# Optimization experiments

Hardware: AMD Instinct MI355X
Metric: run time of the kernel (lower is better)

## Reference

```python
import jax, jax.numpy as jnp
import numpy as np

B, S, D, H = 128, 1024, 512, 512


def setup_inputs() -> dict:
    key = jax.random.key(0)
    ks = jax.random.split(key, 8)
    return {
        "input": jax.random.normal(ks[0], (B, D), jnp.float32),
        "context": jax.random.normal(ks[1], (B, S, D), jnp.float32),
        "mask": jax.random.randint(ks[2], (B, S), 0, 2).astype(bool),
        "W_in": jax.random.normal(ks[3], (H, D), jnp.float32) * (1.0 / np.sqrt(D)),
        "b_in": jax.random.normal(ks[4], (H,), jnp.float32) * 0.01,
        "W_ctx": jax.random.normal(ks[5], (H, D), jnp.float32) * (1.0 / np.sqrt(D)),
        "b_ctx": jax.random.normal(ks[6], (H,), jnp.float32) * 0.01,
        "V": jax.random.uniform(ks[7], (H,), jnp.float32, -1.0, 1.0),
    }


def reference(input, context, mask, W_in, b_in, W_ctx, b_ctx, V):
    # inp: [B, H] -> broadcast over S (torch: unsqueeze(2).expand)
    inp = input @ W_in.T + b_in
    # 1x1 Conv1d over permuted context == per-position linear: [B, H, S]
    ctx = jnp.einsum('bsd,hd->bhs', context, W_ctx) + b_ctx[None, :, None]
    # additive (Bahdanau) score: V . tanh(inp + ctx) over H -> [B, S]
    att = jnp.einsum('h,bhs->bs', V, jnp.tanh(inp[:, :, None] + ctx))
    att = jnp.where(mask, -jnp.inf, att)
    alpha = jax.nn.softmax(att, axis=-1)  # [B, S]
    # weighted sum of projected context: [B, H]
    hidden_state = jnp.einsum('bhs,bs->bh', ctx, alpha)
    return (hidden_state, alpha)
```

## Files before the change

### kernel.cpp

```cpp
#include <hip/hip_runtime.h>
#include <math.h>

#define B_ 128
#define S_ 1024
#define D_ 512
#define H_ 512

typedef _Float16 f16x4 __attribute__((ext_vector_type(4)));
typedef _Float16 f16x8 __attribute__((ext_vector_type(8)));
typedef float    f32x4 __attribute__((ext_vector_type(4)));

__global__ void zero_k(float* __restrict__ p, int n) {
    int i = blockIdx.x * 256 + threadIdx.x;
    if (i < n) p[i] = 0.f;
}

__global__ void init2_k(float* __restrict__ att, float* __restrict__ hidden,
                        const float* __restrict__ bc) {
    int i = blockIdx.x * 256 + threadIdx.x;
    if (i < B_ * S_) att[i] = 0.f;
    else if (i < B_ * S_ + B_ * H_) {
        int j = i - B_ * S_;
        hidden[j] = bc[j & (H_ - 1)];
    }
}

__global__ __launch_bounds__(256) void linear_k(const float* __restrict__ X,
                                                const float* __restrict__ W,
                                                const float* __restrict__ bias,
                                                float* __restrict__ out) {
    int idx = blockIdx.x * 256 + threadIdx.x;
    int b = idx >> 9;
    int h = idx & 511;
    const float4* x = (const float4*)(X + (size_t)b * D_);
    const float4* w = (const float4*)(W + (size_t)h * D_);
    float s = 0.f;
#pragma unroll 8
    for (int k = 0; k < D_ / 4; ++k) {
        float4 xv = x[k], wv = w[k];
        s = fmaf(xv.x, wv.x, s);
        s = fmaf(xv.y, wv.y, s);
        s = fmaf(xv.z, wv.z, s);
        s = fmaf(xv.w, wv.w, s);
    }
    out[idx] = s + bias[h];
}

__device__ inline f16x8 cvt8(float4 a, float4 b) {
    f16x8 r;
    r[0] = (_Float16)a.x; r[1] = (_Float16)a.y;
    r[2] = (_Float16)a.z; r[3] = (_Float16)a.w;
    r[4] = (_Float16)b.x; r[5] = (_Float16)b.y;
    r[6] = (_Float16)b.z; r[7] = (_Float16)b.w;
    return r;
}

__device__ inline float fast_tanh(float x) {
    float e = __expf(2.f * x);
    return 1.f - 2.f / (e + 1.f);
}

template <bool WCTX>
__global__ __launch_bounds__(256) void score_mfma(const float* __restrict__ ctx,
                                                  const float* __restrict__ Wc,
                                                  const float* __restrict__ bc,
                                                  const float* __restrict__ Vv,
                                                  const float* __restrict__ inp,
                                                  float* __restrict__ att,
                                                  _Float16* __restrict__ ctxp) {
    __shared__ __align__(16) _Float16 Ah[2][128][32];
    __shared__ __align__(16) _Float16 Bh[2][128][32];
    __shared__ float red[8][128];

    const int tid = threadIdx.x;
    const int s0 = blockIdx.x * 128;
    const int h0 = blockIdx.y * 128;
    const int b  = blockIdx.z;

    const int r0  = tid >> 2;
    const int kg  = tid & 3;
    const int swz = ((kg ^ (r0 & 3)) << 3);

    const int wave = tid >> 6;
    const int lane = tid & 63;
    const int wm = wave >> 1, wn = wave & 1;
    const int l15 = lane & 15, quad = lane >> 4;
    const int rdsw = ((quad ^ (l15 & 3)) << 3);

    const float* Arow0 = Wc  + (size_t)(h0 + r0) * D_ + kg * 8;
    const float* Arow1 = Arow0 + (size_t)64 * D_;
    const float* Brow0 = ctx + ((size_t)b * S_ + s0 + r0) * D_ + kg * 8;
    const float* Brow1 = Brow0 + (size_t)64 * D_;

    f32x4 acc[4][4];
#pragma unroll
    for (int mi = 0; mi < 4; ++mi)
#pragma unroll
        for (int ni = 0; ni < 4; ++ni) acc[mi][ni] = (f32x4){0.f, 0.f, 0.f, 0.f};

    float4 A0a, A0b, A1a, A1b, B0a, B0b, B1a, B1b;

#define LOADS(step) do { const int kk_ = (step) * 32;                               \
    A0a = *(const float4*)(Arow0 + kk_); A0b = *(const float4*)(Arow0 + kk_ + 4);   \
    A1a = *(const float4*)(Arow1 + kk_); A1b = *(const float4*)(Arow1 + kk_ + 4);   \
    B0a = *(const float4*)(Brow0 + kk_); B0b = *(const float4*)(Brow0 + kk_ + 4);   \
    B1a = *(const float4*)(Brow1 + kk_); B1b = *(const float4*)(Brow1 + kk_ + 4); } while (0)

#define WRITE(bf) do {                                                              \
    *(f16x8*)&Ah[bf][r0][swz]      = cvt8(A0a, A0b);                                \
    *(f16x8*)&Ah[bf][r0 + 64][swz] = cvt8(A1a, A1b);                                \
    *(f16x8*)&Bh[bf][r0][swz]      = cvt8(B0a, B0b);                                \
    *(f16x8*)&Bh[bf][r0 + 64][swz] = cvt8(B1a, B1b); } while (0)

#define COMPUTE(bf) do {                                                            \
    f16x8 bhf_[4];                                                                  \
    _Pragma("unroll")                                                               \
    for (int ni = 0; ni < 4; ++ni)                                                  \
        bhf_[ni] = *(const f16x8*)&Bh[bf][wn * 64 + ni * 16 + l15][rdsw];           \
    _Pragma("unroll")                                                               \
    for (int mi = 0; mi < 4; ++mi) {                                                \
        f16x8 ah_ = *(const f16x8*)&Ah[bf][wm * 64 + mi * 16 + l15][rdsw];          \
        _Pragma("unroll")                                                           \
        for (int ni = 0; ni < 4; ++ni)                                              \
            acc[mi][ni] = __builtin_amdgcn_mfma_f32_16x16x32_f16(ah_, bhf_[ni],     \
                                                                 acc[mi][ni], 0, 0, 0); \
    } } while (0)

    LOADS(0);
    WRITE(0);
    LOADS(1);
    __syncthreads();

    for (int it = 0; it < 16; it += 2) {
        COMPUTE(0);
        WRITE(1);
        if (it + 2 < 16) LOADS(it + 2);
        __syncthreads();
        COMPUTE(1);
        if (it + 2 < 16) WRITE(0);
        if (it + 3 < 16) LOADS(it + 3);
        __syncthreads();
    }
#undef LOADS
#undef WRITE
#undef COMPUTE

    if (WCTX) {
#pragma unroll
        for (int ni = 0; ni < 4; ++ni) {
            const size_t srow = ((size_t)b * S_ + s0 + wn * 64 + ni * 16 + l15) * H_;
#pragma unroll
            for (int mi = 0; mi < 4; ++mi) {
                f16x4 v;
                v[0] = (_Float16)acc[mi][ni][0];
                v[1] = (_Float16)acc[mi][ni][1];
                v[2] = (_Float16)acc[mi][ni][2];
                v[3] = (_Float16)acc[mi][ni][3];
                *(f16x4*)(ctxp + srow + h0 + wm * 64 + mi * 16 + quad * 4) = v;
            }
        }
    }

    float p[4] = {0.f, 0.f, 0.f, 0.f};
#pragma unroll
    for (int mi = 0; mi < 4; ++mi) {
#pragma unroll
        for (int r = 0; r < 4; ++r) {
            const int h = h0 + wm * 64 + mi * 16 + quad * 4 + r;
            const float c  = inp[(size_t)b * H_ + h] + bc[h];
            const float vh = Vv[h];
#pragma unroll
            for (int ni = 0; ni < 4; ++ni)
                p[ni] = fmaf(vh, fast_tanh(c + acc[mi][ni][r]), p[ni]);
        }
    }
    const int cid = wm * 4 + quad;
#pragma unroll
    for (int ni = 0; ni < 4; ++ni)
        red[cid][wn * 64 + ni * 16 + l15] = p[ni];
    __syncthreads();
    if (tid < 128) {
        float s = 0.f;
#pragma unroll
        for (int g = 0; g < 8; ++g) s += red[g][tid];
        atomicAdd(att + (size_t)b * S_ + s0 + tid, s);
    }
}

__global__ __launch_bounds__(256) void softmax_k(const float* __restrict__ att,
                                                 const int* __restrict__ mask,
                                                 float* __restrict__ alpha) {
    const int b = blockIdx.x;
    const int t = threadIdx.x;
    __shared__ float sm[256];
    float v[4];
    float mx = -INFINITY;
#pragma unroll
    for (int i = 0; i < 4; ++i) {
        int s = t + i * 256;
        float a = att[(size_t)b * S_ + s];
        int mk = mask[(size_t)b * S_ + s];
        v[i] = mk ? -INFINITY : a;
        mx = fmaxf(mx, v[i]);
    }
    sm[t] = mx;
    __syncthreads();
    for (int off = 128; off > 0; off >>= 1) {
        if (t < off) sm[t] = fmaxf(sm[t], sm[t + off]);
        __syncthreads();
    }
    mx = sm[0];
    __syncthreads();
    float e[4];
    float sum = 0.f;
#pragma unroll
    for (int i = 0; i < 4; ++i) {
        e[i] = expf(v[i] - mx);
        sum += e[i];
    }
    sm[t] = sum;
    __syncthreads();
    for (int off = 128; off > 0; off >>= 1) {
        if (t < off) sm[t] += sm[t + off];
        __syncthreads();
    }
    float inv = 1.f / sm[0];
#pragma unroll
    for (int i = 0; i < 4; ++i) alpha[(size_t)b * S_ + t + i * 256] = e[i] * inv;
}

__global__ __launch_bounds__(256) void cbar2_k(const _Float16* __restrict__ ctxp,
                                               const float* __restrict__ alpha,
                                               float* __restrict__ hidden) {
    const int b  = blockIdx.y;
    const int s0 = blockIdx.x * 128;
    const int t  = threadIdx.x;
    const int w = t >> 6, lane = t & 63;
    __shared__ float al[128];
    __shared__ float red[3][512];
    if (t < 128) al[t] = alpha[(size_t)b * S_ + s0 + t];
    __syncthreads();
    const _Float16* base = ctxp + ((size_t)b * S_ + s0) * H_ + lane * 8;
    float acc[8] = {0.f, 0.f, 0.f, 0.f, 0.f, 0.f, 0.f, 0.f};
#pragma unroll 4
    for (int s = w; s < 128; s += 4) {
        float a = al[s];
        f16x8 v = *(const f16x8*)(base + (size_t)s * H_);
#pragma unroll
        for (int j = 0; j < 8; ++j) acc[j] = fmaf(a, (float)v[j], acc[j]);
    }
    if (w > 0) {
#pragma unroll
        for (int j = 0; j < 8; ++j) red[w - 1][lane * 8 + j] = acc[j];
    }
    __syncthreads();
    if (w == 0) {
        float* dst = hidden + (size_t)b * H_ + lane * 8;
#pragma unroll
        for (int j = 0; j < 8; ++j)
            atomicAdd(dst + j, acc[j] + red[0][lane * 8 + j] + red[1][lane * 8 + j] + red[2][lane * 8 + j]);
    }
}

__global__ __launch_bounds__(256) void cbar_k(const float* __restrict__ ctx,
                                              const float* __restrict__ alpha,
                                              float* __restrict__ cbar) {
    const int b = blockIdx.y;
    const int s0 = blockIdx.x * 128;
    const int t = threadIdx.x;
    const int c4 = t & 127;
    const int sh = t >> 7;
    __shared__ float al[128];
    __shared__ float4 red[128];
    if (t < 128) al[t] = alpha[(size_t)b * S_ + s0 + t];
    __syncthreads();
    const float4* base = (const float4*)(ctx + ((size_t)b * S_ + s0) * D_);
    float4 c = {0.f, 0.f, 0.f, 0.f};
#pragma unroll 4
    for (int s = sh; s < 128; s += 2) {
        float a = al[s];
        float4 x = base[(size_t)s * (D_ / 4) + c4];
        c.x = fmaf(a, x.x, c.x);
        c.y = fmaf(a, x.y, c.y);
        c.z = fmaf(a, x.z, c.z);
        c.w = fmaf(a, x.w, c.w);
    }
    if (sh == 1) red[c4] = c;
    __syncthreads();
    if (sh == 0) {
        float4 o = red[c4];
        float* dst = cbar + (size_t)b * D_ + c4 * 4;
        atomicAdd(dst + 0, c.x + o.x);
        atomicAdd(dst + 1, c.y + o.y);
        atomicAdd(dst + 2, c.z + o.z);
        atomicAdd(dst + 3, c.w + o.w);
    }
}

extern "C" void kernel_launch(void* const* d_in, const int* in_sizes, int n_in,
                              void* d_out, int out_size, void* d_ws, size_t ws_size,
                              hipStream_t stream) {
    const float* input = (const float*)d_in[0];
    const float* ctx   = (const float*)d_in[1];
    const int*   mask  = (const int*)d_in[2];
    const float* W_in  = (const float*)d_in[3];
    const float* b_in  = (const float*)d_in[4];
    const float* W_ctx = (const float*)d_in[5];
    const float* b_ctx = (const float*)d_in[6];
    const float* V     = (const float*)d_in[7];

    float* hidden = (float*)d_out;
    float* alpha  = (float*)d_out + B_ * H_;

    float* inp  = (float*)d_ws;
    float* att  = inp + B_ * H_;
    float* cbar = att + B_ * S_;
    _Float16* ctxp = (_Float16*)(cbar + B_ * D_);

    const size_t base_bytes = (size_t)(B_ * H_ + B_ * S_ + B_ * D_) * sizeof(float);
    const size_t ctxp_bytes = (size_t)B_ * S_ * H_ * sizeof(_Float16);
    const bool big = ws_size >= base_bytes + ctxp_bytes;

    dim3 g2(S_ / 128, H_ / 128, B_);

    if (big) {
        int ni = B_ * S_ + B_ * H_;
        init2_k<<<(ni + 255) / 256, 256, 0, stream>>>(att, hidden, b_ctx);

        linear_k<<<(B_ * H_) / 256, 256, 0, stream>>>(input, W_in, b_in, inp);

        score_mfma<true><<<g2, 256, 0, stream>>>(ctx, W_ctx, b_ctx, V, inp, att, ctxp);

        softmax_k<<<B_, 256, 0, stream>>>(att, mask, alpha);

        dim3 g4(S_ / 128, B_);
        cbar2_k<<<g4, 256, 0, stream>>>(ctxp, alpha, hidden);
    } else {
        int nz = B_ * S_ + B_ * D_;
        zero_k<<<(nz + 255) / 256, 256, 0, stream>>>(att, nz);

        linear_k<<<(B_ * H_) / 256, 256, 0, stream>>>(input, W_in, b_in, inp);

        score_mfma<false><<<g2, 256, 0, stream>>>(ctx, W_ctx, b_ctx, V, inp, att, nullptr);

        softmax_k<<<B_, 256, 0, stream>>>(att, mask, alpha);

        dim3 g4(S_ / 128, B_);
        cbar_k<<<g4, 256, 0, stream>>>(ctx, alpha, cbar);

        linear_k<<<(B_ * H_) / 256, 256, 0, stream>>>(cbar, W_ctx, b_ctx, hidden);
    }
}
```

Measured before the change: 554.0 us.

## Pre-convert context and W_ctx to fp16, stage via global_load_lds in score kernel

```diff
diff --git a/kernel.cpp b/kernel.cpp
--- a/kernel.cpp
+++ b/kernel.cpp
@@ -10,18 +10,32 @@
 typedef _Float16 f16x8 __attribute__((ext_vector_type(8)));
 typedef float    f32x4 __attribute__((ext_vector_type(4)));
 
+#if defined(__has_builtin)
+#if __has_builtin(__builtin_amdgcn_global_load_lds)
+#define HAVE_GLDS 1
+#endif
+#endif
+#ifndef HAVE_GLDS
+#define HAVE_GLDS 0
+#endif
+
 __global__ void zero_k(float* __restrict__ p, int n) {
     int i = blockIdx.x * 256 + threadIdx.x;
     if (i < n) p[i] = 0.f;
 }
 
-__global__ void init2_k(float* __restrict__ att, float* __restrict__ hidden,
-                        const float* __restrict__ bc) {
+__global__ __launch_bounds__(256) void cvt16_k(const float* __restrict__ src,
+                                               _Float16* __restrict__ dst, int n8) {
     int i = blockIdx.x * 256 + threadIdx.x;
-    if (i < B_ * S_) att[i] = 0.f;
-    else if (i < B_ * S_ + B_ * H_) {
-        int j = i - B_ * S_;
-        hidden[j] = bc[j & (H_ - 1)];
+    if (i < n8) {
+        float4 a = ((const float4*)src)[2 * i];
+        float4 b = ((const float4*)src)[2 * i + 1];
+        f16x8 r;
+        r[0] = (_Float16)a.x; r[1] = (_Float16)a.y;
+        r[2] = (_Float16)a.z; r[3] = (_Float16)a.w;
+        r[4] = (_Float16)b.x; r[5] = (_Float16)b.y;
+        r[6] = (_Float16)b.z; r[7] = (_Float16)b.w;
+        *(f16x8*)(dst + (size_t)8 * i) = r;
     }
 }
 
@@ -60,14 +74,111 @@
     return 1.f - 2.f / (e + 1.f);
 }
 
-template <bool WCTX>
-__global__ __launch_bounds__(256) void score_mfma(const float* __restrict__ ctx,
-                                                  const float* __restrict__ Wc,
-                                                  const float* __restrict__ bc,
-                                                  const float* __restrict__ Vv,
-                                                  const float* __restrict__ inp,
-                                                  float* __restrict__ att,
-                                                  _Float16* __restrict__ ctxp) {
+__device__ inline void stage16(const _Float16* g, _Float16* l, int lane) {
+#if HAVE_GLDS
+    __builtin_amdgcn_global_load_lds((__attribute__((address_space(1))) void*)g,
+                                     (__attribute__((address_space(3))) void*)l,
+                                     16, 0, 0);
+#else
+    f16x8 v = *(const f16x8*)g;
+    *(f16x8*)((char*)l + lane * 16) = v;
+#endif
+}
+
+__global__ __launch_bounds__(256) void score16(const _Float16* __restrict__ ctx16,
+                                               const _Float16* __restrict__ Wc16,
+                                               const float* __restrict__ bc,
+                                               const float* __restrict__ Vv,
+                                               const float* __restrict__ inp,
+                                               float* __restrict__ att) {
+    __shared__ __align__(16) _Float16 Ah[2][128][32];
+    __shared__ __align__(16) _Float16 Bh[2][128][32];
+    __shared__ float red[8][128];
+
+    const int tid = threadIdx.x;
+    const int s0 = blockIdx.x * 128;
+    const int h0 = blockIdx.y * 128;
+    const int b  = blockIdx.z;
+
+    const int wave = tid >> 6;
+    const int lane = tid & 63;
+    const int wm = wave >> 1, wn = wave & 1;
+    const int l15 = lane & 15, quad = lane >> 4;
+
+    const int rrow = lane >> 2;
+    const int rgr  = lane & 3;
+    const _Float16* Ag = Wc16 + (size_t)(h0 + wave * 32 + rrow) * D_ + rgr * 8;
+    const _Float16* Bg = ctx16 + ((size_t)b * S_ + s0 + wave * 32 + rrow) * D_ + rgr * 8;
+
+    f32x4 acc[4][4];
+#pragma unroll
+    for (int mi = 0; mi < 4; ++mi)
+#pragma unroll
+        for (int ni = 0; ni < 4; ++ni) acc[mi][ni] = (f32x4){0.f, 0.f, 0.f, 0.f};
+
+#define STAGE(bf, k0) do {                                                      \
+    stage16(Ag + (k0),            &Ah[bf][wave * 32][0],      lane);            \
+    stage16(Ag + (k0) + 16 * D_,  &Ah[bf][wave * 32 + 16][0], lane);            \
+    stage16(Bg + (k0),            &Bh[bf][wave * 32][0],      lane);            \
+    stage16(Bg + (k0) + 16 * D_,  &Bh[bf][wave * 32 + 16][0], lane); } while (0)
+
+#define COMPUTE(bf) do {                                                        \
+    f16x8 bhf_[4];                                                              \
+    _Pragma("unroll")                                                           \
+    for (int ni = 0; ni < 4; ++ni)                                              \
+        bhf_[ni] = *(const f16x8*)&Bh[bf][wn * 64 + ni * 16 + l15][quad * 8];   \
+    _Pragma("unroll")                                                           \
+    for (int mi = 0; mi < 4; ++mi) {                                            \
+        f16x8 ah_ = *(const f16x8*)&Ah[bf][wm * 64 + mi * 16 + l15][quad * 8];  \
+        _Pragma("unroll")                                                       \
+        for (int ni = 0; ni < 4; ++ni)                                          \
+            acc[mi][ni] = __builtin_amdgcn_mfma_f32_16x16x32_f16(ah_, bhf_[ni], \
+                                                                 acc[mi][ni], 0, 0, 0); \
+    } } while (0)
+
+    STAGE(0, 0);
+    __syncthreads();
+#pragma unroll
+    for (int it = 0; it < 16; ++it) {
+        if (it + 1 < 16) STAGE((it + 1) & 1, (it + 1) * 32);
+        COMPUTE(it & 1);
+        __syncthreads();
+    }
+#undef STAGE
+#undef COMPUTE
+
+    float p[4] = {0.f, 0.f, 0.f, 0.f};
+#pragma unroll
+    for (int mi = 0; mi < 4; ++mi) {
+#pragma unroll
+        for (int r = 0; r < 4; ++r) {
+            const int h = h0 + wm * 64 + mi * 16 + quad * 4 + r;
+            const float c  = inp[(size_t)b * H_ + h] + bc[h];
+            const float vh = Vv[h];
+#pragma unroll
+            for (int ni = 0; ni < 4; ++ni)
+                p[ni] = fmaf(vh, fast_tanh(c + acc[mi][ni][r]), p[ni]);
+        }
+    }
+    const int cid = wm * 4 + quad;
+#pragma unroll
+    for (int ni = 0; ni < 4; ++ni)
+        red[cid][wn * 64 + ni * 16 + l15] = p[ni];
+    __syncthreads();
+    if (tid < 128) {
+        float s = 0.f;
+#pragma unroll
+        for (int g = 0; g < 8; ++g) s += red[g][tid];
+        atomicAdd(att + (size_t)b * S_ + s0 + tid, s);
+    }
+}
+
+__global__ __launch_bounds__(256) void score_f32(const float* __restrict__ ctx,
+                                                 const float* __restrict__ Wc,
+                                                 const float* __restrict__ bc,
+                                                 const float* __restrict__ Vv,
+                                                 const float* __restrict__ inp,
+                                                 float* __restrict__ att) {
     __shared__ __align__(16) _Float16 Ah[2][128][32];
     __shared__ __align__(16) _Float16 Bh[2][128][32];
     __shared__ float red[8][128];
@@ -145,22 +256,6 @@
 #undef WRITE
 #undef COMPUTE
 
-    if (WCTX) {
-#pragma unroll
-        for (int ni = 0; ni < 4; ++ni) {
-            const size_t srow = ((size_t)b * S_ + s0 + wn * 64 + ni * 16 + l15) * H_;
-#pragma unroll
-            for (int mi = 0; mi < 4; ++mi) {
-                f16x4 v;
-                v[0] = (_Float16)acc[mi][ni][0];
-                v[1] = (_Float16)acc[mi][ni][1];
-                v[2] = (_Float16)acc[mi][ni][2];
-                v[3] = (_Float16)acc[mi][ni][3];
-                *(f16x4*)(ctxp + srow + h0 + wm * 64 + mi * 16 + quad * 4) = v;
-            }
-        }
-    }
-
     float p[4] = {0.f, 0.f, 0.f, 0.f};
 #pragma unroll
     for (int mi = 0; mi < 4; ++mi) {
@@ -229,9 +324,9 @@
     for (int i = 0; i < 4; ++i) alpha[(size_t)b * S_ + t + i * 256] = e[i] * inv;
 }
 
-__global__ __launch_bounds__(256) void cbar2_k(const _Float16* __restrict__ ctxp,
+__global__ __launch_bounds__(256) void cbarh_k(const _Float16* __restrict__ src16,
                                                const float* __restrict__ alpha,
-                                               float* __restrict__ hidden) {
+                                               float* __restrict__ out) {
     const int b  = blockIdx.y;
     const int s0 = blockIdx.x * 128;
     const int t  = threadIdx.x;
@@ -240,12 +335,12 @@
     __shared__ float red[3][512];
     if (t < 128) al[t] = alpha[(size_t)b * S_ + s0 + t];
     __syncthreads();
-    const _Float16* base = ctxp + ((size_t)b * S_ + s0) * H_ + lane * 8;
+    const _Float16* base = src16 + ((size_t)b * S_ + s0) * D_ + lane * 8;
     float acc[8] = {0.f, 0.f, 0.f, 0.f, 0.f, 0.f, 0.f, 0.f};
 #pragma unroll 4
     for (int s = w; s < 128; s += 4) {
         float a = al[s];
-        f16x8 v = *(const f16x8*)(base + (size_t)s * H_);
+        f16x8 v = *(const f16x8*)(base + (size_t)s * D_);
 #pragma unroll
         for (int j = 0; j < 8; ++j) acc[j] = fmaf(a, (float)v[j], acc[j]);
     }
@@ -255,7 +350,7 @@
     }
     __syncthreads();
     if (w == 0) {
-        float* dst = hidden + (size_t)b * H_ + lane * 8;
+        float* dst = out + (size_t)b * D_ + lane * 8;
 #pragma unroll
         for (int j = 0; j < 8; ++j)
             atomicAdd(dst + j, acc[j] + red[0][lane * 8 + j] + red[1][lane * 8 + j] + red[2][lane * 8 + j]);
@@ -315,37 +410,41 @@
     float* inp  = (float*)d_ws;
     float* att  = inp + B_ * H_;
     float* cbar = att + B_ * S_;
-    _Float16* ctxp = (_Float16*)(cbar + B_ * D_);
+    _Float16* ctx16 = (_Float16*)(cbar + B_ * D_);
+    _Float16* Wc16  = ctx16 + (size_t)B_ * S_ * D_;
 
     const size_t base_bytes = (size_t)(B_ * H_ + B_ * S_ + B_ * D_) * sizeof(float);
-    const size_t ctxp_bytes = (size_t)B_ * S_ * H_ * sizeof(_Float16);
-    const bool big = ws_size >= base_bytes + ctxp_bytes;
+    const size_t f16_bytes  = ((size_t)B_ * S_ * D_ + (size_t)H_ * D_) * sizeof(_Float16);
+    const bool big = ws_size >= base_bytes + f16_bytes;
 
     dim3 g2(S_ / 128, H_ / 128, B_);
+    dim3 g4(S_ / 128, B_);
+    const int nz = B_ * S_ + B_ * D_;
 
     if (big) {
-        int ni = B_ * S_ + B_ * H_;
-        init2_k<<<(ni + 255) / 256, 256, 0, stream>>>(att, hidden, b_ctx);
+        zero_k<<<(nz + 255) / 256, 256, 0, stream>>>(att, nz);
+
+        cvt16_k<<<(B_ * S_ * D_ / 8 + 255) / 256, 256, 0, stream>>>(ctx, ctx16, B_ * S_ * D_ / 8);
+        cvt16_k<<<(H_ * D_ / 8 + 255) / 256, 256, 0, stream>>>(W_ctx, Wc16, H_ * D_ / 8);
 
         linear_k<<<(B_ * H_) / 256, 256, 0, stream>>>(input, W_in, b_in, inp);
 
-        score_mfma<true><<<g2, 256, 0, stream>>>(ctx, W_ctx, b_ctx, V, inp, att, ctxp);
+        score16<<<g2, 256, 0, stream>>>(ctx16, Wc16, b_ctx, V, inp, att);
 
         softmax_k<<<B_, 256, 0, stream>>>(att, mask, alpha);
 
-        dim3 g4(S_ / 128, B_);
-        cbar2_k<<<g4, 256, 0, stream>>>(ctxp, alpha, hidden);
+        cbarh_k<<<g4, 256, 0, stream>>>(ctx16, alpha, cbar);
+
+        linear_k<<<(B_ * H_) / 256, 256, 0, stream>>>(cbar, W_ctx, b_ctx, hidden);
     } else {
-        int nz = B_ * S_ + B_ * D_;
         zero_k<<<(nz + 255) / 256, 256, 0, stream>>>(att, nz);
 
         linear_k<<<(B_ * H_) / 256, 256, 0, stream>>>(input, W_in, b_in, inp);
 
-        score_mfma<false><<<g2, 256, 0, stream>>>(ctx, W_ctx, b_ctx, V, inp, att, nullptr);
+        score_f32<<<g2, 256, 0, stream>>>(ctx, W_ctx, b_ctx, V, inp, att);
 
         softmax_k<<<B_, 256, 0, stream>>>(att, mask, alpha);
 
-        dim3 g4(S_ / 128, B_);
         cbar_k<<<g4, 256, 0, stream>>>(ctx, alpha, cbar);
 
         linear_k<<<(B_ * H_) / 256, 256, 0, stream>>>(cbar, W_ctx, b_ctx, hidden);
```

After: 570.2 us. +2.9%, slower.
